# Kernel optimization log

Measured on AMD Instinct MI355X. Metric: run time of the kernel, lower is better.

Reference implementation:

```python
import jax, jax.numpy as jnp
import numpy as np

B, S, IN, OUT = 4, 2048, 4096, 4096


def setup_inputs() -> dict:
    key = jax.random.key(0)
    k_x, k_w, k_s, k_b = jax.random.split(key, 4)
    x = jax.random.normal(k_x, (B, S, IN), dtype=jnp.float16)
    # int8 quantized weight, layout [in_features, out_features] (torch.t(weight) in __init__)
    w_q = jax.random.randint(k_w, (IN, OUT), -128, 128, dtype=jnp.int32).astype(jnp.int8)
    # per-output-channel dequant scale (typical w8 per-channel scale magnitude)
    scale = (jax.random.uniform(k_s, (OUT,), dtype=jnp.float32) * 0.02 + 0.001).astype(jnp.float16)
    bias = jax.random.normal(k_b, (OUT,), dtype=jnp.float16)
    return {"x": x, "w_q": w_q, "scale": scale, "bias": bias}


def reference(x, w_q, scale, bias):
    # w8_a16_gemm: inline dequant int8 -> fp16 via per-column scale, then GEMM in fp16
    w = w_q.astype(jnp.float16) * scale[None, :]          # [in, out]
    out = jnp.einsum('bsi,io->bso', x, w)                 # [B, S, out]
    return out + bias
```

## Files before the change

kernel.cpp:

```cpp
#include <hip/hip_runtime.h>
#include <stdint.h>


typedef __attribute__((ext_vector_type(4))) float     f32x4;
typedef __attribute__((ext_vector_type(8))) _Float16  f16x8;

#define M_DIM 8192
#define N_DIM 4096
#define K_DIM 4096

__global__ __launch_bounds__(256) void convert_x_to_f16(const float* __restrict__ x,
                                                        _Float16* __restrict__ Xh) {
    const size_t i = ((size_t)blockIdx.x * 256 + threadIdx.x) * 8;
    float4 v0 = *(const float4*)(x + i);
    float4 v1 = *(const float4*)(x + i + 4);
    f16x8 h;
    h[0] = (_Float16)v0.x; h[1] = (_Float16)v0.y; h[2] = (_Float16)v0.z; h[3] = (_Float16)v0.w;
    h[4] = (_Float16)v1.x; h[5] = (_Float16)v1.y; h[6] = (_Float16)v1.z; h[7] = (_Float16)v1.w;
    *(f16x8*)(Xh + i) = h;
}

__global__ __launch_bounds__(256) void dequant_w_to_f16(const int* __restrict__ wq,
                                                        _Float16* __restrict__ Wt) {
    __shared__ _Float16 tile[64][65];
    const int n0 = blockIdx.x * 64;
    const int k0 = blockIdx.y * 64;
    const int t  = threadIdx.x;
    const int r  = t >> 2;
    const int c0 = (t & 3) * 16;
    const int* src = wq + (size_t)(k0 + r) * N_DIM + n0 + c0;
#pragma unroll
    for (int j = 0; j < 4; ++j) {
        int4 q = *(const int4*)(src + j * 4);
        tile[c0 + j * 4 + 0][r] = (_Float16)q.x;
        tile[c0 + j * 4 + 1][r] = (_Float16)q.y;
        tile[c0 + j * 4 + 2][r] = (_Float16)q.z;
        tile[c0 + j * 4 + 3][r] = (_Float16)q.w;
    }
    __syncthreads();
    const int nn  = t >> 2;
    const int cc0 = (t & 3) * 16;
    _Float16 vals[16] __attribute__((aligned(16)));
#pragma unroll
    for (int j = 0; j < 16; ++j) vals[j] = tile[nn][cc0 + j];
    _Float16* dst = Wt + (size_t)(n0 + nn) * K_DIM + k0 + cc0;
    *(float4*)(dst + 0) = *(const float4*)(vals + 0);
    *(float4*)(dst + 8) = *(const float4*)(vals + 8);
}

#define AS1C(p) (const __attribute__((address_space(1))) void*)(p)
#define AS3C(p) (__attribute__((address_space(3))) void*)(p)

#define STAGE_A(arr, h, tile) do {                                                    \
    __builtin_amdgcn_global_load_lds(                                                 \
        AS1C(aStageBase + (size_t)((h) * 128) * K_DIM + (tile) * 64),                 \
        AS3C((char*)(arr) + (h) * 16384 + t * 16), 16, 0, 0);                         \
    __builtin_amdgcn_global_load_lds(                                                 \
        AS1C(aStageBase + (size_t)((h) * 128 + 64) * K_DIM + (tile) * 64),            \
        AS3C((char*)(arr) + (h) * 16384 + 8192 + t * 16), 16, 0, 0);                  \
} while (0)

#define STAGE_B(arr, h, tile) do {                                                    \
    __builtin_amdgcn_global_load_lds(                                                 \
        AS1C(bStageBase + (size_t)((h) * 128) * K_DIM + (tile) * 64),                 \
        AS3C((char*)(arr) + (h) * 16384 + t * 16), 16, 0, 0);                         \
    __builtin_amdgcn_global_load_lds(                                                 \
        AS1C(bStageBase + (size_t)((h) * 128 + 64) * K_DIM + (tile) * 64),            \
        AS3C((char*)(arr) + (h) * 16384 + 8192 + t * 16), 16, 0, 0);                  \
} while (0)

#define DSR(dst, addr, IMM) \
    asm volatile("ds_read_b128 %0, %1 offset:%c2" : "=v"(dst) : "v"(addr), "i"(IMM))

#define DSRA(S, Q, A0, A1)                   \
    DSR(S[0][0], A0, (Q) * 4096);            \
    DSR(S[0][1], A1, (Q) * 4096);            \
    DSR(S[1][0], A0, (Q) * 4096 + 2048);     \
    DSR(S[1][1], A1, (Q) * 4096 + 2048)

#define DSRB(BA0, BA1)                       \
    DSR(bf[0][0], BA0, 0);    DSR(bf[0][1], BA1, 0);    \
    DSR(bf[1][0], BA0, 2048); DSR(bf[1][1], BA1, 2048); \
    DSR(bf[2][0], BA0, 4096); DSR(bf[2][1], BA1, 4096); \
    DSR(bf[3][0], BA0, 6144); DSR(bf[3][1], BA1, 6144)

#define MMS(S, AI, N)                                                                 \
    acc[AI][N] = __builtin_amdgcn_mfma_f32_16x16x32_f16(S[(AI) & 1][0], bf[N][0],     \
                                                        acc[AI][N], 0, 0, 0);         \
    acc[AI][N] = __builtin_amdgcn_mfma_f32_16x16x32_f16(S[(AI) & 1][1], bf[N][1],     \
                                                        acc[AI][N], 0, 0, 0)

#define MFMA16(Q, S)                                                  \
    MMS(S, (Q) * 2 + 0, 0); MMS(S, (Q) * 2 + 0, 1);                   \
    MMS(S, (Q) * 2 + 0, 2); MMS(S, (Q) * 2 + 0, 3);                   \
    MMS(S, (Q) * 2 + 1, 0); MMS(S, (Q) * 2 + 1, 1);                   \
    MMS(S, (Q) * 2 + 1, 2); MMS(S, (Q) * 2 + 1, 3)

#define BARR()  __builtin_amdgcn_s_barrier()
#define SB0()   __builtin_amdgcn_sched_barrier(0)
#define LGKM0() do { asm volatile("s_waitcnt lgkmcnt(0)" ::: "memory"); SB0(); } while (0)
#define LGKM4() do { asm volatile("s_waitcnt lgkmcnt(4)" ::: "memory"); SB0(); } while (0)
#define VMC2()  asm volatile("s_waitcnt vmcnt(2)" ::: "memory")
#define PRIO1() __builtin_amdgcn_s_setprio(1)
#define PRIO0() __builtin_amdgcn_s_setprio(0)

#define KTILE(A0, A1, B0, B1, Adst, Bdst, tl) do {                                    \
    STAGE_A(Adst, 0, tl);                        \
    VMC2();                                       \
    BARR();                                              \
    DSRB(B0, B1);                                                                     \
    DSRA(aq0, 0, A0, A1);                                                             \
    DSRA(aq1, 1, A0, A1);                                                             \
    LGKM4();  PRIO1(); MFMA16(0, aq0); PRIO0();                                       \
    DSRA(aq0, 2, A0, A1);  STAGE_A(Adst, 1, tl);                                      \
    LGKM4();  PRIO1(); MFMA16(1, aq1); PRIO0();                                       \
    DSRA(aq1, 3, A0, A1);  STAGE_B(Bdst, 0, tl);                                      \
    LGKM4();  PRIO1(); MFMA16(2, aq0); PRIO0();                                       \
    STAGE_B(Bdst, 1, tl);                                                             \
    LGKM0();  PRIO1(); MFMA16(3, aq1); PRIO0();                                       \
    BARR();                                     \
} while (0)

__global__ __launch_bounds__(512, 2) void gemm_8phase(const _Float16* __restrict__ Xh,
                                                      const _Float16* __restrict__ Wt,
                                                      const float* __restrict__ scale,
                                                      const float* __restrict__ bias,
                                                      float* __restrict__ C) {
    __shared__ __attribute__((aligned(128))) _Float16 As0_[16384];
    __shared__ __attribute__((aligned(128))) _Float16 As1_[16384];
    __shared__ __attribute__((aligned(128))) _Float16 Bs0_[16384];
    __shared__ __attribute__((aligned(128))) _Float16 Bs1_[16384];

    const int bid = blockIdx.x;
    const int swz = (bid & 7) * 64 + (bid >> 3);
    const int bm  = swz >> 4;
    const int bn  = swz & 15;

    const int t  = threadIdx.x;
    const int l  = t & 63;
    const int w  = t >> 6;
    const int wm = w >> 2, wn = w & 3;
    const int lr = l & 15, lh = l >> 4;

    const int rowIdx = t >> 3;
    const int kbSw   = ((t & 7) * 16) ^ ((rowIdx & 7) << 4);
    const _Float16* aStageBase = Xh + (size_t)(bm * 256 + rowIdx) * K_DIM + (kbSw >> 1);
    const _Float16* bStageBase = Wt + (size_t)(bn * 256 + rowIdx) * K_DIM + (kbSw >> 1);

    const int  mask = (lr & 7) << 4;
    const uint32_t m6   = (uint32_t)(mask & 64);
    const uint32_t aoff = (uint32_t)((wm * 128 + lr) * 128 + ((lh * 16) ^ (mask & 48)));
    const uint32_t boff = (uint32_t)((wn * 64 + lr) * 128 + ((lh * 16) ^ (mask & 48)));
    const uint32_t aA0k0 = (uint32_t)(uintptr_t)As0_ + aoff + m6;
    const uint32_t aA0k1 = (uint32_t)(uintptr_t)As0_ + aoff + (64u ^ m6);
    const uint32_t aA1k0 = (uint32_t)(uintptr_t)As1_ + aoff + m6;
    const uint32_t aA1k1 = (uint32_t)(uintptr_t)As1_ + aoff + (64u ^ m6);
    const uint32_t bB0k0 = (uint32_t)(uintptr_t)Bs0_ + boff + m6;
    const uint32_t bB0k1 = (uint32_t)(uintptr_t)Bs0_ + boff + (64u ^ m6);
    const uint32_t bB1k0 = (uint32_t)(uintptr_t)Bs1_ + boff + m6;
    const uint32_t bB1k1 = (uint32_t)(uintptr_t)Bs1_ + boff + (64u ^ m6);

    f16x8 aq0[2][2], aq1[2][2], bf[4][2];
    f32x4 acc[8][4] = {};

    STAGE_A(As0_, 0, 0); STAGE_A(As0_, 1, 0);
    STAGE_B(Bs0_, 0, 0); STAGE_B(Bs0_, 1, 0);

#pragma unroll 1
    for (int i = 0; i < K_DIM / 128; ++i) {
        const int t1 = 2 * i + 1;
        const int t2 = (2 * i + 2) & 63;
        KTILE(aA0k0, aA0k1, bB0k0, bB0k1, As1_, Bs1_, t1);
        KTILE(aA1k0, aA1k1, bB1k0, bB1k1, As0_, Bs0_, t2);
    }
    asm volatile("s_waitcnt vmcnt(0)" ::: "memory");

    const int col0 = bn * 256 + wn * 64 + lr;
    const int row0 = bm * 256 + wm * 128 + lh * 4;
    float sc[4], bi[4];
#pragma unroll
    for (int ni = 0; ni < 4; ++ni) {
        sc[ni] = scale[col0 + ni * 16];
        bi[ni] = bias[col0 + ni * 16];
    }
#pragma unroll
    for (int ai = 0; ai < 8; ++ai)
#pragma unroll
        for (int r = 0; r < 4; ++r) {
            const size_t rowOff = (size_t)(row0 + ai * 16 + r) * N_DIM;
#pragma unroll
            for (int ni = 0; ni < 4; ++ni)
                C[rowOff + col0 + ni * 16] = acc[ai][ni][r] * sc[ni] + bi[ni];
        }
}

extern "C" void kernel_launch(void* const* d_in, const int* in_sizes, int n_in,
                              void* d_out, int out_size, void* d_ws, size_t ws_size,
                              hipStream_t stream) {
    const float* x     = (const float*)d_in[0];
    const int*   wq    = (const int*)d_in[1];
    const float* scale = (const float*)d_in[2];
    const float* bias  = (const float*)d_in[3];
    float* out = (float*)d_out;

    const size_t needW = (size_t)N_DIM * K_DIM * sizeof(_Float16);
    _Float16* Wt = (_Float16*)d_ws;
    _Float16* Xh = (_Float16*)((char*)d_ws + needW);

    dim3 tgrid(N_DIM / 64, K_DIM / 64);
    dequant_w_to_f16<<<tgrid, 256, 0, stream>>>(wq, Wt);
    convert_x_to_f16<<<((size_t)M_DIM * K_DIM) / (256 * 8), 256, 0, stream>>>(x, Xh);

    const int nblocks = (M_DIM / 256) * (N_DIM / 256);
    gemm_8phase<<<nblocks, 512, 0, stream>>>(Xh, Wt, scale, bias, out);
}
```

Measured before the change: 274.0 us.

## Switch GEMM inner loop from 16x16x32 to 32x32x16 MFMA tiles

Replaces the 16x16x32 f16 MFMA micro-kernel with 32x32x16 MFMAs, so each wave computes its 128x64 tile as 4x2 blocks of 32x32 instead of 8x4 blocks of 16x16. The LDS read addressing, fragment registers and epilogue row/column mapping are rebuilt for the 32x32 output layout. The aim is fewer LDS fragment reads and MFMA issues per K-step, since larger MFMA tiles reuse each operand more. The wait counts and swizzle offsets are rewritten to match, which risks new bank conflicts or stalls in the pipelined schedule.

```diff
diff --git a/kernel.cpp b/kernel.cpp
--- a/kernel.cpp
+++ b/kernel.cpp
@@ -2,7 +2,7 @@
 #include <stdint.h>
 
 
-typedef __attribute__((ext_vector_type(4))) float     f32x4;
+typedef __attribute__((ext_vector_type(16))) float    f32x16;
 typedef __attribute__((ext_vector_type(8))) _Float16  f16x8;
 
 #define M_DIM 8192
@@ -72,60 +72,51 @@
 #define DSR(dst, addr, IMM) \
     asm volatile("ds_read_b128 %0, %1 offset:%c2" : "=v"(dst) : "v"(addr), "i"(IMM))
 
-#define DSRA(S, Q, A0, A1)                   \
-    DSR(S[0][0], A0, (Q) * 4096);            \
-    DSR(S[0][1], A1, (Q) * 4096);            \
-    DSR(S[1][0], A0, (Q) * 4096 + 2048);     \
-    DSR(S[1][1], A1, (Q) * 4096 + 2048)
-
-#define DSRB(BA0, BA1)                       \
-    DSR(bf[0][0], BA0, 0);    DSR(bf[0][1], BA1, 0);    \
-    DSR(bf[1][0], BA0, 2048); DSR(bf[1][1], BA1, 2048); \
-    DSR(bf[2][0], BA0, 4096); DSR(bf[2][1], BA1, 4096); \
-    DSR(bf[3][0], BA0, 6144); DSR(bf[3][1], BA1, 6144)
-
-#define MMS(S, AI, N)                                                                 \
-    acc[AI][N] = __builtin_amdgcn_mfma_f32_16x16x32_f16(S[(AI) & 1][0], bf[N][0],     \
-                                                        acc[AI][N], 0, 0, 0);         \
-    acc[AI][N] = __builtin_amdgcn_mfma_f32_16x16x32_f16(S[(AI) & 1][1], bf[N][1],     \
-                                                        acc[AI][N], 0, 0, 0)
-
-#define MFMA16(Q, S)                                                  \
-    MMS(S, (Q) * 2 + 0, 0); MMS(S, (Q) * 2 + 0, 1);                   \
-    MMS(S, (Q) * 2 + 0, 2); MMS(S, (Q) * 2 + 0, 3);                   \
-    MMS(S, (Q) * 2 + 1, 0); MMS(S, (Q) * 2 + 1, 1);                   \
-    MMS(S, (Q) * 2 + 1, 2); MMS(S, (Q) * 2 + 1, 3)
+#define DSRK(S, aA, bA)                      \
+    DSR(afr##S[0], aA, 0);                   \
+    DSR(afr##S[1], aA, 4096);                \
+    DSR(afr##S[2], aA, 8192);                \
+    DSR(afr##S[3], aA, 12288);               \
+    DSR(bfr##S[0], bA, 0);                   \
+    DSR(bfr##S[1], bA, 4096)
+
+#define MM32(S, AI, BI)                                                               \
+    acc[AI][BI] = __builtin_amdgcn_mfma_f32_32x32x16_f16(afr##S[AI], bfr##S[BI],      \
+                                                         acc[AI][BI], 0, 0, 0)
+
+#define MFMA8(S)                                                      \
+    MM32(S, 0, 0); MM32(S, 0, 1); MM32(S, 1, 0); MM32(S, 1, 1);       \
+    MM32(S, 2, 0); MM32(S, 2, 1); MM32(S, 3, 0); MM32(S, 3, 1)
 
 #define BARR()  __builtin_amdgcn_s_barrier()
 #define SB0()   __builtin_amdgcn_sched_barrier(0)
 #define LGKM0() do { asm volatile("s_waitcnt lgkmcnt(0)" ::: "memory"); SB0(); } while (0)
-#define LGKM4() do { asm volatile("s_waitcnt lgkmcnt(4)" ::: "memory"); SB0(); } while (0)
+#define LGKM6() do { asm volatile("s_waitcnt lgkmcnt(6)" ::: "memory"); SB0(); } while (0)
 #define VMC2()  asm volatile("s_waitcnt vmcnt(2)" ::: "memory")
 #define PRIO1() __builtin_amdgcn_s_setprio(1)
 #define PRIO0() __builtin_amdgcn_s_setprio(0)
 
-#define KTILE(A0, A1, B0, B1, Adst, Bdst, tl) do {                                    \
+#define KTILE(aAd, bAd, Adst, Bdst, tl) do {                                          \
     STAGE_A(Adst, 0, tl);                        \
     VMC2();                                       \
     BARR();                                              \
-    DSRB(B0, B1);                                                                     \
-    DSRA(aq0, 0, A0, A1);                                                             \
-    DSRA(aq1, 1, A0, A1);                                                             \
-    LGKM4();  PRIO1(); MFMA16(0, aq0); PRIO0();                                       \
-    DSRA(aq0, 2, A0, A1);  STAGE_A(Adst, 1, tl);                                      \
-    LGKM4();  PRIO1(); MFMA16(1, aq1); PRIO0();                                       \
-    DSRA(aq1, 3, A0, A1);  STAGE_B(Bdst, 0, tl);                                      \
-    LGKM4();  PRIO1(); MFMA16(2, aq0); PRIO0();                                       \
+    DSRK(0, aAd[0], bAd[0]);                                                          \
+    DSRK(1, aAd[1], bAd[1]);                                                          \
+    LGKM6();  PRIO1(); MFMA8(0); PRIO0();                                             \
+    DSRK(0, aAd[2], bAd[2]);  STAGE_A(Adst, 1, tl);                                   \
+    LGKM6();  PRIO1(); MFMA8(1); PRIO0();                                             \
+    DSRK(1, aAd[3], bAd[3]);  STAGE_B(Bdst, 0, tl);                                   \
+    LGKM6();  PRIO1(); MFMA8(0); PRIO0();                                             \
     STAGE_B(Bdst, 1, tl);                                                             \
-    LGKM0();  PRIO1(); MFMA16(3, aq1); PRIO0();                                       \
+    LGKM0();  PRIO1(); MFMA8(1); PRIO0();                                             \
     BARR();                                     \
 } while (0)
 
-__global__ __launch_bounds__(512, 2) void gemm_8phase(const _Float16* __restrict__ Xh,
-                                                      const _Float16* __restrict__ Wt,
-                                                      const float* __restrict__ scale,
-                                                      const float* __restrict__ bias,
-                                                      float* __restrict__ C) {
+__global__ __launch_bounds__(512, 2) void gemm_mb32(const _Float16* __restrict__ Xh,
+                                                    const _Float16* __restrict__ Wt,
+                                                    const float* __restrict__ scale,
+                                                    const float* __restrict__ bias,
+                                                    float* __restrict__ C) {
     __shared__ __attribute__((aligned(128))) _Float16 As0_[16384];
     __shared__ __attribute__((aligned(128))) _Float16 As1_[16384];
     __shared__ __attribute__((aligned(128))) _Float16 Bs0_[16384];
@@ -140,28 +131,29 @@
     const int l  = t & 63;
     const int w  = t >> 6;
     const int wm = w >> 2, wn = w & 3;
-    const int lr = l & 15, lh = l >> 4;
 
     const int rowIdx = t >> 3;
     const int kbSw   = ((t & 7) * 16) ^ ((rowIdx & 7) << 4);
     const _Float16* aStageBase = Xh + (size_t)(bm * 256 + rowIdx) * K_DIM + (kbSw >> 1);
     const _Float16* bStageBase = Wt + (size_t)(bn * 256 + rowIdx) * K_DIM + (kbSw >> 1);
 
-    const int  mask = (lr & 7) << 4;
-    const uint32_t m6   = (uint32_t)(mask & 64);
-    const uint32_t aoff = (uint32_t)((wm * 128 + lr) * 128 + ((lh * 16) ^ (mask & 48)));
-    const uint32_t boff = (uint32_t)((wn * 64 + lr) * 128 + ((lh * 16) ^ (mask & 48)));
-    const uint32_t aA0k0 = (uint32_t)(uintptr_t)As0_ + aoff + m6;
-    const uint32_t aA0k1 = (uint32_t)(uintptr_t)As0_ + aoff + (64u ^ m6);
-    const uint32_t aA1k0 = (uint32_t)(uintptr_t)As1_ + aoff + m6;
-    const uint32_t aA1k1 = (uint32_t)(uintptr_t)As1_ + aoff + (64u ^ m6);
-    const uint32_t bB0k0 = (uint32_t)(uintptr_t)Bs0_ + boff + m6;
-    const uint32_t bB0k1 = (uint32_t)(uintptr_t)Bs0_ + boff + (64u ^ m6);
-    const uint32_t bB1k0 = (uint32_t)(uintptr_t)Bs1_ + boff + m6;
-    const uint32_t bB1k1 = (uint32_t)(uintptr_t)Bs1_ + boff + (64u ^ m6);
-
-    f16x8 aq0[2][2], aq1[2][2], bf[4][2];
-    f32x4 acc[8][4] = {};
+    const int col32 = l & 31;
+    const int kh16  = (l >> 5) * 16;
+    const int mask7 = (l & 7) << 4;
+    const uint32_t aRowOff = (uint32_t)((wm * 128 + col32) * 128);
+    const uint32_t bRowOff = (uint32_t)((wn * 64 + col32) * 128);
+    uint32_t aAd0[4], aAd1[4], bAd0[4], bAd1[4];
+#pragma unroll
+    for (int ks = 0; ks < 4; ++ks) {
+        const uint32_t bk = (uint32_t)((ks * 32 + kh16) ^ mask7);
+        aAd0[ks] = (uint32_t)(uintptr_t)As0_ + aRowOff + bk;
+        aAd1[ks] = (uint32_t)(uintptr_t)As1_ + aRowOff + bk;
+        bAd0[ks] = (uint32_t)(uintptr_t)Bs0_ + bRowOff + bk;
+        bAd1[ks] = (uint32_t)(uintptr_t)Bs1_ + bRowOff + bk;
+    }
+
+    f16x8 afr0[4], afr1[4], bfr0[2], bfr1[2];
+    f32x16 acc[4][2] = {};
 
     STAGE_A(As0_, 0, 0); STAGE_A(As0_, 1, 0);
     STAGE_B(Bs0_, 0, 0); STAGE_B(Bs0_, 1, 0);
@@ -170,28 +162,29 @@
     for (int i = 0; i < K_DIM / 128; ++i) {
         const int t1 = 2 * i + 1;
         const int t2 = (2 * i + 2) & 63;
-        KTILE(aA0k0, aA0k1, bB0k0, bB0k1, As1_, Bs1_, t1);
-        KTILE(aA1k0, aA1k1, bB1k0, bB1k1, As0_, Bs0_, t2);
+        KTILE(aAd0, bAd0, As1_, Bs1_, t1);
+        KTILE(aAd1, bAd1, As0_, Bs0_, t2);
     }
     asm volatile("s_waitcnt vmcnt(0)" ::: "memory");
 
-    const int col0 = bn * 256 + wn * 64 + lr;
-    const int row0 = bm * 256 + wm * 128 + lh * 4;
-    float sc[4], bi[4];
-#pragma unroll
-    for (int ni = 0; ni < 4; ++ni) {
-        sc[ni] = scale[col0 + ni * 16];
-        bi[ni] = bias[col0 + ni * 16];
-    }
-#pragma unroll
-    for (int ai = 0; ai < 8; ++ai)
-#pragma unroll
-        for (int r = 0; r < 4; ++r) {
-            const size_t rowOff = (size_t)(row0 + ai * 16 + r) * N_DIM;
-#pragma unroll
-            for (int ni = 0; ni < 4; ++ni)
-                C[rowOff + col0 + ni * 16] = acc[ai][ni][r] * sc[ni] + bi[ni];
-        }
+    const int colBase = bn * 256 + wn * 64 + col32;
+    const int rowBase = bm * 256 + wm * 128 + 4 * (l >> 5);
+    float sc[2], bi[2];
+#pragma unroll
+    for (int b2 = 0; b2 < 2; ++b2) {
+        sc[b2] = scale[colBase + b2 * 32];
+        bi[b2] = bias[colBase + b2 * 32];
+    }
+#pragma unroll
+    for (int am = 0; am < 4; ++am)
+#pragma unroll
+        for (int b2 = 0; b2 < 2; ++b2)
+#pragma unroll
+            for (int reg = 0; reg < 16; ++reg) {
+                const int row = rowBase + am * 32 + (reg & 3) + 8 * (reg >> 2);
+                C[(size_t)row * N_DIM + colBase + b2 * 32] =
+                    acc[am][b2][reg] * sc[b2] + bi[b2];
+            }
 }
 
 extern "C" void kernel_launch(void* const* d_in, const int* in_sizes, int n_in,
@@ -212,5 +205,5 @@
     convert_x_to_f16<<<((size_t)M_DIM * K_DIM) / (256 * 8), 256, 0, stream>>>(x, Xh);
 
     const int nblocks = (M_DIM / 256) * (N_DIM / 256);
-    gemm_8phase<<<nblocks, 512, 0, stream>>>(Xh, Wt, scale, bias, out);
-}
+    gemm_mb32<<<nblocks, 512, 0, stream>>>(Xh, Wt, scale, bias, out);
+}
```

Result: slower. 299.1 us (+9.2%).

## Use 16 waves per block with 64x64 warp tiles for GEMM

Applied to the files above, without the earlier changes.

Doubles the workgroup to 1024 threads (16 waves in a 4x4 grid) so each wave computes a 64x64 output tile instead of 128x64, halving per-wave accumulators. Each thread now issues one async global-to-LDS load per half-tile instead of two, and the fine-grained interleaving of LDS reads, staging and MFMA groups is replaced by a simpler schedule: issue all staging loads up front, then two rounds of 8 LDS reads followed by 16 MFMAs. The launch bounds of (1024, 4) ask for four such blocks per CU, which the 128KB of LDS per block cannot fit. Each LDS-resident operand is now read by more waves, and the simpler schedule gives up some overlap of LDS reads with MFMA work.

```diff
diff --git a/kernel.cpp b/kernel.cpp
--- a/kernel.cpp
+++ b/kernel.cpp
@@ -51,81 +51,62 @@
 #define AS1C(p) (const __attribute__((address_space(1))) void*)(p)
 #define AS3C(p) (__attribute__((address_space(3))) void*)(p)
 
-#define STAGE_A(arr, h, tile) do {                                                    \
+#define STAGE_A(arr, h, tile)                                                         \
     __builtin_amdgcn_global_load_lds(                                                 \
         AS1C(aStageBase + (size_t)((h) * 128) * K_DIM + (tile) * 64),                 \
-        AS3C((char*)(arr) + (h) * 16384 + t * 16), 16, 0, 0);                         \
-    __builtin_amdgcn_global_load_lds(                                                 \
-        AS1C(aStageBase + (size_t)((h) * 128 + 64) * K_DIM + (tile) * 64),            \
-        AS3C((char*)(arr) + (h) * 16384 + 8192 + t * 16), 16, 0, 0);                  \
-} while (0)
+        AS3C((char*)(arr) + (h) * 16384 + t * 16), 16, 0, 0)
 
-#define STAGE_B(arr, h, tile) do {                                                    \
+#define STAGE_B(arr, h, tile)                                                         \
     __builtin_amdgcn_global_load_lds(                                                 \
         AS1C(bStageBase + (size_t)((h) * 128) * K_DIM + (tile) * 64),                 \
-        AS3C((char*)(arr) + (h) * 16384 + t * 16), 16, 0, 0);                         \
-    __builtin_amdgcn_global_load_lds(                                                 \
-        AS1C(bStageBase + (size_t)((h) * 128 + 64) * K_DIM + (tile) * 64),            \
-        AS3C((char*)(arr) + (h) * 16384 + 8192 + t * 16), 16, 0, 0);                  \
-} while (0)
+        AS3C((char*)(arr) + (h) * 16384 + t * 16), 16, 0, 0)
 
 #define DSR(dst, addr, IMM) \
     asm volatile("ds_read_b128 %0, %1 offset:%c2" : "=v"(dst) : "v"(addr), "i"(IMM))
 
-#define DSRA(S, Q, A0, A1)                   \
-    DSR(S[0][0], A0, (Q) * 4096);            \
-    DSR(S[0][1], A1, (Q) * 4096);            \
-    DSR(S[1][0], A0, (Q) * 4096 + 2048);     \
-    DSR(S[1][1], A1, (Q) * 4096 + 2048)
+#define DSR8(aK, bK)            \
+    DSR(a0, aK, 0);             \
+    DSR(a1, aK, 2048);          \
+    DSR(a2, aK, 4096);          \
+    DSR(a3, aK, 6144);          \
+    DSR(b0, bK, 0);             \
+    DSR(b1, bK, 2048);          \
+    DSR(b2, bK, 4096);          \
+    DSR(b3, bK, 6144)
 
-#define DSRB(BA0, BA1)                       \
-    DSR(bf[0][0], BA0, 0);    DSR(bf[0][1], BA1, 0);    \
-    DSR(bf[1][0], BA0, 2048); DSR(bf[1][1], BA1, 2048); \
-    DSR(bf[2][0], BA0, 4096); DSR(bf[2][1], BA1, 4096); \
-    DSR(bf[3][0], BA0, 6144); DSR(bf[3][1], BA1, 6144)
+#define MM(AI, NI, AV, BV) \
+    acc[AI][NI] = __builtin_amdgcn_mfma_f32_16x16x32_f16(AV, BV, acc[AI][NI], 0, 0, 0)
 
-#define MMS(S, AI, N)                                                                 \
-    acc[AI][N] = __builtin_amdgcn_mfma_f32_16x16x32_f16(S[(AI) & 1][0], bf[N][0],     \
-                                                        acc[AI][N], 0, 0, 0);         \
-    acc[AI][N] = __builtin_amdgcn_mfma_f32_16x16x32_f16(S[(AI) & 1][1], bf[N][1],     \
-                                                        acc[AI][N], 0, 0, 0)
-
-#define MFMA16(Q, S)                                                  \
-    MMS(S, (Q) * 2 + 0, 0); MMS(S, (Q) * 2 + 0, 1);                   \
-    MMS(S, (Q) * 2 + 0, 2); MMS(S, (Q) * 2 + 0, 3);                   \
-    MMS(S, (Q) * 2 + 1, 0); MMS(S, (Q) * 2 + 1, 1);                   \
-    MMS(S, (Q) * 2 + 1, 2); MMS(S, (Q) * 2 + 1, 3)
+#define MFMA16()                                                      \
+    MM(0, 0, a0, b0); MM(0, 1, a0, b1); MM(0, 2, a0, b2); MM(0, 3, a0, b3); \
+    MM(1, 0, a1, b0); MM(1, 1, a1, b1); MM(1, 2, a1, b2); MM(1, 3, a1, b3); \
+    MM(2, 0, a2, b0); MM(2, 1, a2, b1); MM(2, 2, a2, b2); MM(2, 3, a2, b3); \
+    MM(3, 0, a3, b0); MM(3, 1, a3, b1); MM(3, 2, a3, b2); MM(3, 3, a3, b3)
 
 #define BARR()  __builtin_amdgcn_s_barrier()
 #define SB0()   __builtin_amdgcn_sched_barrier(0)
 #define LGKM0() do { asm volatile("s_waitcnt lgkmcnt(0)" ::: "memory"); SB0(); } while (0)
-#define LGKM4() do { asm volatile("s_waitcnt lgkmcnt(4)" ::: "memory"); SB0(); } while (0)
-#define VMC2()  asm volatile("s_waitcnt vmcnt(2)" ::: "memory")
+#define VMC4()  asm volatile("s_waitcnt vmcnt(4)" ::: "memory")
 #define PRIO1() __builtin_amdgcn_s_setprio(1)
 #define PRIO0() __builtin_amdgcn_s_setprio(0)
 
-#define KTILE(A0, A1, B0, B1, Adst, Bdst, tl) do {                                    \
-    STAGE_A(Adst, 0, tl);                        \
-    VMC2();                                       \
-    BARR();                                              \
-    DSRB(B0, B1);                                                                     \
-    DSRA(aq0, 0, A0, A1);                                                             \
-    DSRA(aq1, 1, A0, A1);                                                             \
-    LGKM4();  PRIO1(); MFMA16(0, aq0); PRIO0();                                       \
-    DSRA(aq0, 2, A0, A1);  STAGE_A(Adst, 1, tl);                                      \
-    LGKM4();  PRIO1(); MFMA16(1, aq1); PRIO0();                                       \
-    DSRA(aq1, 3, A0, A1);  STAGE_B(Bdst, 0, tl);                                      \
-    LGKM4();  PRIO1(); MFMA16(2, aq0); PRIO0();                                       \
-    STAGE_B(Bdst, 1, tl);                                                             \
-    LGKM0();  PRIO1(); MFMA16(3, aq1); PRIO0();                                       \
-    BARR();                                     \
+#define KTILE(aK0, aK1, bK0, bK1, Adst, Bdst, tl) do {                                \
+    STAGE_A(Adst, 0, tl); STAGE_A(Adst, 1, tl);                                       \
+    STAGE_B(Bdst, 0, tl); STAGE_B(Bdst, 1, tl);                                       \
+    VMC4();                                      \
+    BARR();                                                   \
+    DSR8(aK0, bK0);                                                                   \
+    LGKM0(); PRIO1(); MFMA16(); PRIO0();                                              \
+    DSR8(aK1, bK1);                                                                   \
+    LGKM0(); PRIO1(); MFMA16(); PRIO0();                                              \
+    BARR();                                      \
 } while (0)
 
-__global__ __launch_bounds__(512, 2) void gemm_8phase(const _Float16* __restrict__ Xh,
-                                                      const _Float16* __restrict__ Wt,
-                                                      const float* __restrict__ scale,
-                                                      const float* __restrict__ bias,
-                                                      float* __restrict__ C) {
+__global__ __launch_bounds__(1024, 4) void gemm_w16(const _Float16* __restrict__ Xh,
+                                                    const _Float16* __restrict__ Wt,
+                                                    const float* __restrict__ scale,
+                                                    const float* __restrict__ bias,
+                                                    float* __restrict__ C) {
     __shared__ __attribute__((aligned(128))) _Float16 As0_[16384];
     __shared__ __attribute__((aligned(128))) _Float16 As1_[16384];
     __shared__ __attribute__((aligned(128))) _Float16 Bs0_[16384];
@@ -149,7 +130,7 @@
 
     const int  mask = (lr & 7) << 4;
     const uint32_t m6   = (uint32_t)(mask & 64);
-    const uint32_t aoff = (uint32_t)((wm * 128 + lr) * 128 + ((lh * 16) ^ (mask & 48)));
+    const uint32_t aoff = (uint32_t)((wm * 64 + lr) * 128 + ((lh * 16) ^ (mask & 48)));
     const uint32_t boff = (uint32_t)((wn * 64 + lr) * 128 + ((lh * 16) ^ (mask & 48)));
     const uint32_t aA0k0 = (uint32_t)(uintptr_t)As0_ + aoff + m6;
     const uint32_t aA0k1 = (uint32_t)(uintptr_t)As0_ + aoff + (64u ^ m6);
@@ -160,8 +141,8 @@
     const uint32_t bB1k0 = (uint32_t)(uintptr_t)Bs1_ + boff + m6;
     const uint32_t bB1k1 = (uint32_t)(uintptr_t)Bs1_ + boff + (64u ^ m6);
 
-    f16x8 aq0[2][2], aq1[2][2], bf[4][2];
-    f32x4 acc[8][4] = {};
+    f16x8 a0, a1, a2, a3, b0, b1, b2, b3;
+    f32x4 acc[4][4] = {};
 
     STAGE_A(As0_, 0, 0); STAGE_A(As0_, 1, 0);
     STAGE_B(Bs0_, 0, 0); STAGE_B(Bs0_, 1, 0);
@@ -176,7 +157,7 @@
     asm volatile("s_waitcnt vmcnt(0)" ::: "memory");
 
     const int col0 = bn * 256 + wn * 64 + lr;
-    const int row0 = bm * 256 + wm * 128 + lh * 4;
+    const int row0 = bm * 256 + wm * 64 + lh * 4;
     float sc[4], bi[4];
 #pragma unroll
     for (int ni = 0; ni < 4; ++ni) {
@@ -184,13 +165,13 @@
         bi[ni] = bias[col0 + ni * 16];
     }
 #pragma unroll
-    for (int ai = 0; ai < 8; ++ai)
+    for (int mi = 0; mi < 4; ++mi)
 #pragma unroll
         for (int r = 0; r < 4; ++r) {
-            const size_t rowOff = (size_t)(row0 + ai * 16 + r) * N_DIM;
+            const size_t rowOff = (size_t)(row0 + mi * 16 + r) * N_DIM;
 #pragma unroll
             for (int ni = 0; ni < 4; ++ni)
-                C[rowOff + col0 + ni * 16] = acc[ai][ni][r] * sc[ni] + bi[ni];
+                C[rowOff + col0 + ni * 16] = acc[mi][ni][r] * sc[ni] + bi[ni];
         }
 }
 
@@ -212,5 +193,5 @@
     convert_x_to_f16<<<((size_t)M_DIM * K_DIM) / (256 * 8), 256, 0, stream>>>(x, Xh);
 
     const int nblocks = (M_DIM / 256) * (N_DIM / 256);
-    gemm_8phase<<<nblocks, 512, 0, stream>>>(Xh, Wt, scale, bias, out);
+    gemm_w16<<<nblocks, 1024, 0, stream>>>(Xh, Wt, scale, bias, out);
 }
```

Measured after the change: 290.9 us. 6.1% more time.

## Fuse fp32-to-fp16 activation conversion into GEMM register-staged A loads

Applied to the files above, without the earlier changes.

Drops the separate x conversion kernel and its fp16 workspace buffer. The GEMM now loads fp32 activations straight into registers, converts them to fp16 and writes them to swizzled LDS, with the next tile's load overlapping the current MFMA phase. This removes one full read and write pass over the activations, but A no longer uses direct global-to-LDS loads, so register pressure goes up and fp32 traffic per GEMM block doubles.

```diff
diff --git a/kernel.cpp b/kernel.cpp
--- a/kernel.cpp
+++ b/kernel.cpp
@@ -8,17 +8,6 @@
 #define M_DIM 8192
 #define N_DIM 4096
 #define K_DIM 4096
-
-__global__ __launch_bounds__(256) void convert_x_to_f16(const float* __restrict__ x,
-                                                        _Float16* __restrict__ Xh) {
-    const size_t i = ((size_t)blockIdx.x * 256 + threadIdx.x) * 8;
-    float4 v0 = *(const float4*)(x + i);
-    float4 v1 = *(const float4*)(x + i + 4);
-    f16x8 h;
-    h[0] = (_Float16)v0.x; h[1] = (_Float16)v0.y; h[2] = (_Float16)v0.z; h[3] = (_Float16)v0.w;
-    h[4] = (_Float16)v1.x; h[5] = (_Float16)v1.y; h[6] = (_Float16)v1.z; h[7] = (_Float16)v1.w;
-    *(f16x8*)(Xh + i) = h;
-}
 
 __global__ __launch_bounds__(256) void dequant_w_to_f16(const int* __restrict__ wq,
                                                         _Float16* __restrict__ Wt) {
@@ -51,15 +40,6 @@
 #define AS1C(p) (const __attribute__((address_space(1))) void*)(p)
 #define AS3C(p) (__attribute__((address_space(3))) void*)(p)
 
-#define STAGE_A(arr, h, tile) do {                                                    \
-    __builtin_amdgcn_global_load_lds(                                                 \
-        AS1C(aStageBase + (size_t)((h) * 128) * K_DIM + (tile) * 64),                 \
-        AS3C((char*)(arr) + (h) * 16384 + t * 16), 16, 0, 0);                         \
-    __builtin_amdgcn_global_load_lds(                                                 \
-        AS1C(aStageBase + (size_t)((h) * 128 + 64) * K_DIM + (tile) * 64),            \
-        AS3C((char*)(arr) + (h) * 16384 + 8192 + t * 16), 16, 0, 0);                  \
-} while (0)
-
 #define STAGE_B(arr, h, tile) do {                                                    \
     __builtin_amdgcn_global_load_lds(                                                 \
         AS1C(bStageBase + (size_t)((h) * 128) * K_DIM + (tile) * 64),                 \
@@ -69,6 +49,24 @@
         AS3C((char*)(arr) + (h) * 16384 + 8192 + t * 16), 16, 0, 0);                  \
 } while (0)
 
+#define LOAD_A(tl) do {                                                               \
+    const float4* ap_ = (const float4*)(aSrc + (size_t)(tl) * 64);                    \
+    _Pragma("unroll")                                                                 \
+    for (int j_ = 0; j_ < 8; ++j_) av[j_] = ap_[j_];                                  \
+} while (0)
+
+#define WRITE_A(P) do {                                                               \
+    _Pragma("unroll")                                                                 \
+    for (int j_ = 0; j_ < 4; ++j_) {                                                  \
+        f16x8 h_;                                                                     \
+        h_[0] = (_Float16)av[2 * j_].x;     h_[1] = (_Float16)av[2 * j_].y;           \
+        h_[2] = (_Float16)av[2 * j_].z;     h_[3] = (_Float16)av[2 * j_].w;           \
+        h_[4] = (_Float16)av[2 * j_ + 1].x; h_[5] = (_Float16)av[2 * j_ + 1].y;       \
+        h_[6] = (_Float16)av[2 * j_ + 1].z; h_[7] = (_Float16)av[2 * j_ + 1].w;       \
+        *(f16x8*)((P) + (((akh4 + j_) * 16) ^ aswz)) = h_;                            \
+    }                                                                                 \
+} while (0)
+
 #define DSR(dst, addr, IMM) \
     asm volatile("ds_read_b128 %0, %1 offset:%c2" : "=v"(dst) : "v"(addr), "i"(IMM))
 
@@ -100,32 +98,33 @@
 #define SB0()   __builtin_amdgcn_sched_barrier(0)
 #define LGKM0() do { asm volatile("s_waitcnt lgkmcnt(0)" ::: "memory"); SB0(); } while (0)
 #define LGKM4() do { asm volatile("s_waitcnt lgkmcnt(4)" ::: "memory"); SB0(); } while (0)
-#define VMC2()  asm volatile("s_waitcnt vmcnt(2)" ::: "memory")
+#define VMC8()  asm volatile("s_waitcnt vmcnt(8)" ::: "memory")
 #define PRIO1() __builtin_amdgcn_s_setprio(1)
 #define PRIO0() __builtin_amdgcn_s_setprio(0)
 
-#define KTILE(A0, A1, B0, B1, Adst, Bdst, tl) do {                                    \
-    STAGE_A(Adst, 0, tl);                        \
-    VMC2();                                       \
-    BARR();                                              \
+#define KTILE(A0, A1, B0, B1, BSTG, AWP, tnB, tnA) do {                               \
+    VMC8(); BARR();                               \
     DSRB(B0, B1);                                                                     \
     DSRA(aq0, 0, A0, A1);                                                             \
     DSRA(aq1, 1, A0, A1);                                                             \
     LGKM4();  PRIO1(); MFMA16(0, aq0); PRIO0();                                       \
-    DSRA(aq0, 2, A0, A1);  STAGE_A(Adst, 1, tl);                                      \
+    DSRA(aq0, 2, A0, A1);                                                             \
     LGKM4();  PRIO1(); MFMA16(1, aq1); PRIO0();                                       \
-    DSRA(aq1, 3, A0, A1);  STAGE_B(Bdst, 0, tl);                                      \
+    DSRA(aq1, 3, A0, A1);  STAGE_B(BSTG, 0, tnB);                                     \
     LGKM4();  PRIO1(); MFMA16(2, aq0); PRIO0();                                       \
-    STAGE_B(Bdst, 1, tl);                                                             \
+    STAGE_B(BSTG, 1, tnB);                                                            \
     LGKM0();  PRIO1(); MFMA16(3, aq1); PRIO0();                                       \
-    BARR();                                     \
-} while (0)
-
-__global__ __launch_bounds__(512, 2) void gemm_8phase(const _Float16* __restrict__ Xh,
-                                                      const _Float16* __restrict__ Wt,
-                                                      const float* __restrict__ scale,
-                                                      const float* __restrict__ bias,
-                                                      float* __restrict__ C) {
+    WRITE_A(AWP);                                         \
+    LOAD_A(tnA);                                                \
+    LGKM0();                                                 \
+    BARR();                                                \
+} while (0)
+
+__global__ __launch_bounds__(512, 2) void gemm_fa(const float* __restrict__ x,
+                                                  const _Float16* __restrict__ Wt,
+                                                  const float* __restrict__ scale,
+                                                  const float* __restrict__ bias,
+                                                  float* __restrict__ C) {
     __shared__ __attribute__((aligned(128))) _Float16 As0_[16384];
     __shared__ __attribute__((aligned(128))) _Float16 As1_[16384];
     __shared__ __attribute__((aligned(128))) _Float16 Bs0_[16384];
@@ -142,10 +141,15 @@
     const int wm = w >> 2, wn = w & 3;
     const int lr = l & 15, lh = l >> 4;
 
-    const int rowIdx = t >> 3;
-    const int kbSw   = ((t & 7) * 16) ^ ((rowIdx & 7) << 4);
-    const _Float16* aStageBase = Xh + (size_t)(bm * 256 + rowIdx) * K_DIM + (kbSw >> 1);
-    const _Float16* bStageBase = Wt + (size_t)(bn * 256 + rowIdx) * K_DIM + (kbSw >> 1);
+    const int rowIdxB = t >> 3;
+    const int kbSwB   = ((t & 7) * 16) ^ ((rowIdxB & 7) << 4);
+    const _Float16* bStageBase = Wt + (size_t)(bn * 256 + rowIdxB) * K_DIM + (kbSwB >> 1);
+
+    const int arow = t >> 1, akh = t & 1, akh4 = akh * 4;
+    const int aswz = (arow & 7) << 4;
+    const float* aSrc = x + (size_t)(bm * 256 + arow) * K_DIM + akh * 32;
+    char* a0p = (char*)As0_ + arow * 128;
+    char* a1p = (char*)As1_ + arow * 128;
 
     const int  mask = (lr & 7) << 4;
     const uint32_t m6   = (uint32_t)(mask & 64);
@@ -161,17 +165,22 @@
     const uint32_t bB1k1 = (uint32_t)(uintptr_t)Bs1_ + boff + (64u ^ m6);
 
     f16x8 aq0[2][2], aq1[2][2], bf[4][2];
+    float4 av[8];
     f32x4 acc[8][4] = {};
 
-    STAGE_A(As0_, 0, 0); STAGE_A(As0_, 1, 0);
+    LOAD_A(0);
+    WRITE_A(a0p);
     STAGE_B(Bs0_, 0, 0); STAGE_B(Bs0_, 1, 0);
+    LOAD_A(1);
+    LGKM0();
 
 #pragma unroll 1
-    for (int i = 0; i < K_DIM / 128; ++i) {
-        const int t1 = 2 * i + 1;
-        const int t2 = (2 * i + 2) & 63;
-        KTILE(aA0k0, aA0k1, bB0k0, bB0k1, As1_, Bs1_, t1);
-        KTILE(aA1k0, aA1k1, bB1k0, bB1k1, As0_, Bs0_, t2);
+    for (int it = 0; it < 32; ++it) {
+        const int t1 = 2 * it + 1;
+        const int t2 = (2 * it + 2) & 63;
+        const int t3 = (2 * it + 3) & 63;
+        KTILE(aA0k0, aA0k1, bB0k0, bB0k1, Bs1_, a1p, t1, t2);
+        KTILE(aA1k0, aA1k1, bB1k0, bB1k1, Bs0_, a0p, t2, t3);
     }
     asm volatile("s_waitcnt vmcnt(0)" ::: "memory");
 
@@ -203,14 +212,10 @@
     const float* bias  = (const float*)d_in[3];
     float* out = (float*)d_out;
 
-    const size_t needW = (size_t)N_DIM * K_DIM * sizeof(_Float16);
     _Float16* Wt = (_Float16*)d_ws;
-    _Float16* Xh = (_Float16*)((char*)d_ws + needW);
-
     dim3 tgrid(N_DIM / 64, K_DIM / 64);
     dequant_w_to_f16<<<tgrid, 256, 0, stream>>>(wq, Wt);
-    convert_x_to_f16<<<((size_t)M_DIM * K_DIM) / (256 * 8), 256, 0, stream>>>(x, Xh);
 
     const int nblocks = (M_DIM / 256) * (N_DIM / 256);
-    gemm_8phase<<<nblocks, 512, 0, stream>>>(Xh, Wt, scale, bias, out);
+    gemm_fa<<<nblocks, 512, 0, stream>>>(x, Wt, scale, bias, out);
 }
```

New measurement: 473.2 us. 72.7% more time.
